# Optimization experiments

Hardware: AMD Instinct MI355X
Metric: run time of the kernel (lower is better)

The kernel has to match this reference:

```python
import jax, jax.numpy as jnp
import numpy as np

S, B = 512, 256          # seq_len, batch
A = 16                   # action_size
HID = 64                 # fc hidden_size
R = 256                  # LSTM hidden
IN = HID + A + 1         # LSTM input dim = 81


def setup_inputs() -> dict:
    key = jax.random.key(0)
    ks = jax.random.split(key, 12)
    sc = lambda fan: 1.0 / np.sqrt(fan)
    return {
        "input_tensor": jax.random.normal(ks[0], (S, B, 4, 4), jnp.float32),
        "last_action": jax.random.randint(ks[1], (S, B, 1), 0, A),
        "reward": jax.random.normal(ks[2], (S, B), jnp.float32),
        "done_flags": jax.random.bernoulli(ks[3], 0.05, (S, B)),
        "hidden_state": jax.random.normal(ks[4], (2, B, R), jnp.float32) * 0.1,
        "fc_w": jax.random.normal(ks[5], (HID, 16), jnp.float32) * sc(16),
        "fc_b": jnp.zeros((HID,), jnp.float32),
        "w_ih": jax.random.normal(ks[6], (4 * R, IN), jnp.float32) * sc(R),
        "w_hh": jax.random.normal(ks[7], (4 * R, R), jnp.float32) * sc(R),
        "b_ih": jnp.zeros((4 * R,), jnp.float32),
        "b_hh": jnp.zeros((4 * R,), jnp.float32),
        "actor_w": jax.random.normal(ks[8], (A, R), jnp.float32) * sc(R),
        "actor_b": jnp.zeros((A,), jnp.float32),
        "critic_w": jax.random.normal(ks[9], (1, R), jnp.float32) * sc(R),
        "critic_b": jnp.zeros((1,), jnp.float32),
    }


def reference(input_tensor, last_action, reward, done_flags, hidden_state,
              fc_w, fc_b, w_ih, w_hh, b_ih, b_hh,
              actor_w, actor_b, critic_w, critic_b):
    N = S * B
    # fc over flattened per-step state, then concat [fc_out, reward, one_hot(action)]
    x = input_tensor.reshape(N, 16) @ fc_w.T + fc_b                    # [N, 64]
    onehot = jax.nn.one_hot(last_action.reshape(N), A, dtype=x.dtype)  # [N, 16]
    x = jnp.concatenate([x, reward.reshape(N, 1), onehot], axis=1)     # [N, 81]
    x = x.reshape(S, B, IN)

    def step(carry, xd):
        h, c = carry                       # [B, 256] each
        xt, d = xd                          # [B, 81], [B] bool
        mask = d[:, None]
        h = jnp.where(mask, 0.0, h)         # done-flag state reset
        c = jnp.where(mask, 0.0, c)
        gates = xt @ w_ih.T + b_ih + h @ w_hh.T + b_hh   # [B, 1024]
        i, f, g, o = jnp.split(gates, 4, axis=1)          # torch LSTMCell gate order
        c = jax.nn.sigmoid(f) * c + jax.nn.sigmoid(i) * jnp.tanh(g)
        h = jax.nn.sigmoid(o) * jnp.tanh(c)
        return (h, c), h

    _, hs = jax.lax.scan(step, (hidden_state[0], hidden_state[1]), (x, done_flags))
    hs = hs.reshape(N, R)                                 # == torch.cat(lstm_outputs, 0)
    logits = hs @ actor_w.T + actor_b                     # [N, A]
    values = hs @ critic_w.T + critic_b                   # [N, 1]
    return logits.reshape(S, A, B), values.reshape(S, B)
```

## Files before the change

kernel.cpp:

```cpp
#include <hip/hip_runtime.h>
#include <hip/hip_bf16.h>

#define NS 512
#define NB 256
#define NA 16
#define NR_ 256

typedef short s16x8 __attribute__((ext_vector_type(8)));
typedef float f32x4 __attribute__((ext_vector_type(4)));

union BU { uint4 u4; unsigned short us[8]; s16x8 v; unsigned long long ull[2]; };

__device__ __forceinline__ float bf2f(unsigned short h){
  unsigned u = ((unsigned)h) << 16;
  return __builtin_bit_cast(float, u);
}
__device__ __forceinline__ unsigned short f2bf(float f){
  unsigned u = __builtin_bit_cast(unsigned, f);
  u += 0x7fffu + ((u >> 16) & 1u);
  return (unsigned short)(u >> 16);
}
__device__ __forceinline__ float fsig(float x){ return 1.f/(1.f+__expf(-x)); }
__device__ __forceinline__ float ftanh_(float x){ float e=__expf(2.f*x); return 1.f - 2.f/(e+1.f); }

__global__ void k_detect(const unsigned* __restrict__ done, unsigned* __restrict__ hdr){
  unsigned any = 0;
  for (int i = threadIdx.x; i < 32768; i += 256) any |= (done[i] > 1u) ? 1u : 0u;
  if (__ballot(any)) { if ((threadIdx.x & 63) == 0) atomicOr(hdr, 1u); }
}

__global__ void k_norm(const unsigned char* __restrict__ d8, const int* __restrict__ d32,
                       const unsigned* __restrict__ hdr, unsigned char* __restrict__ dm){
  int i = blockIdx.x*256 + threadIdx.x;
  bool u8 = (hdr[0] & 1u) != 0;
  unsigned char v;
  if (u8) v = (d8[i] != 0) ? 1 : 0; else v = (d32[i] != 0) ? 1 : 0;
  dm[i] = v;
}

__global__ void k_wbprep(const float* __restrict__ w_ih, const float* __restrict__ b_ih,
                         const float* __restrict__ b_hh, unsigned short* __restrict__ wb,
                         float* __restrict__ bsum){
  const int g = blockIdx.x*256 + threadIdx.x;
  bsum[g] = b_ih[g] + b_hh[g];
  const float* src = w_ih + (size_t)g*81;
  unsigned short* dst = wb + (size_t)g*96;
  for (int k=0;k<81;k++) dst[k]=f2bf(src[k]);
  for (int k=81;k<96;k++) dst[k]=0;
}

__global__ void k_wprep2(const float* __restrict__ w_hh, unsigned short* __restrict__ wpack){
  const int G = blockIdx.x*256 + threadIdx.x;
  const int dw  = G >> 12;
  const int rem = G & 4095;
  const int idx = rem >> 6;
  const int c   = rem & 63;
  const int lp = c >> 4, lr = c & 15;
  const int kt = idx >> 3, mt = idx & 7;
  const int grow = ((mt>>1)<<8) + (dw<<5) + ((mt&1)<<4) + lr;
  const int kcol = (kt<<5) + (lp<<3);
  const float* src = w_hh + (size_t)grow*256 + kcol;
  float4 a = *(const float4*)src;
  float4 b = *(const float4*)(src+4);
  BU u;
  u.us[0]=f2bf(a.x); u.us[1]=f2bf(a.y); u.us[2]=f2bf(a.z); u.us[3]=f2bf(a.w);
  u.us[4]=f2bf(b.x); u.us[5]=f2bf(b.y); u.us[6]=f2bf(b.z); u.us[7]=f2bf(b.w);
  *(uint4*)(wpack + (size_t)G*8) = u.u4;
}

__global__ void k_act(const float* __restrict__ input, const float* __restrict__ reward,
                      const int* __restrict__ lastact, const float* __restrict__ fc_w,
                      const float* __restrict__ fc_b, unsigned short* __restrict__ act, int n0){
  __shared__ float wf[1024];
  __shared__ float bfc[64];
  const int tid = threadIdx.x;
  for (int i=tid;i<1024;i+=256) wf[i]=fc_w[i];
  if (tid<64) bfc[tid]=fc_b[tid];
  __syncthreads();
  const int r = blockIdx.x*256 + tid;
  const int n = n0 + r;
  float in[16];
  const float4* ip = (const float4*)(input + (size_t)n*16);
  #pragma unroll
  for (int i=0;i<4;i++){ float4 v=ip[i]; in[4*i]=v.x; in[4*i+1]=v.y; in[4*i+2]=v.z; in[4*i+3]=v.w; }
  unsigned short o[96];
  const float4* wf4=(const float4*)wf;
  #pragma unroll
  for (int q=0;q<64;q++){
    float a=bfc[q];
    #pragma unroll
    for (int k4=0;k4<4;k4++){
      float4 wv=wf4[q*4+k4];
      a += in[4*k4]*wv.x + in[4*k4+1]*wv.y + in[4*k4+2]*wv.z + in[4*k4+3]*wv.w;
    }
    o[q]=f2bf(a);
  }
  o[64]=f2bf(reward[n]);
  const int la = lastact[n];
  #pragma unroll
  for (int k=0;k<16;k++) o[65+k] = (k==la) ? (unsigned short)0x3F80 : (unsigned short)0;
  #pragma unroll
  for (int k=81;k<96;k++) o[k]=0;
  uint4* dst=(uint4*)(act + (size_t)r*96);
  #pragma unroll
  for (int i=0;i<12;i++){
    BU b;
    #pragma unroll
    for (int jj=0;jj<8;jj++) b.us[jj]=o[i*8+jj];
    dst[i]=b.u4;
  }
}

__launch_bounds__(256,1) __global__ void k_gemm(
    const unsigned short* __restrict__ act, const unsigned short* __restrict__ wb,
    const float* __restrict__ bsum, unsigned short* __restrict__ xg, int mtiles){
  __shared__ __align__(16) unsigned short lA[128*104];
  __shared__ __align__(16) unsigned short lB[128*104];
  const int bm = blockIdx.x % mtiles;
  const int bn = blockIdx.x / mtiles;
  const int tid = threadIdx.x;
  {
    const int r = tid >> 1, sg = tid & 1;
    const uint4* sa = (const uint4*)(act + (size_t)(bm*128 + r)*96 + sg*48);
    const uint4* sb = (const uint4*)(wb  + (size_t)(bn*128 + r)*96 + sg*48);
    uint4* da = (uint4*)&lA[r*104 + sg*48];
    uint4* db = (uint4*)&lB[r*104 + sg*48];
    #pragma unroll
    for (int i=0;i<6;i++){ da[i]=sa[i]; db[i]=sb[i]; }
  }
  __syncthreads();
  const int wid = tid >> 6, lane = tid & 63;
  const int wm = wid >> 1, wn = wid & 1;
  const int lr = lane & 15, lp = lane >> 4;
  f32x4 acc[4][4] = {};
  #pragma unroll
  for (int kt=0;kt<3;kt++){
    s16x8 af[4], bf[4];
    #pragma unroll
    for (int mi=0;mi<4;mi++)
      af[mi] = *(const s16x8*)&lA[(wm*64 + mi*16 + lr)*104 + kt*32 + lp*8];
    #pragma unroll
    for (int ni=0;ni<4;ni++)
      bf[ni] = *(const s16x8*)&lB[(wn*64 + ni*16 + lr)*104 + kt*32 + lp*8];
    #pragma unroll
    for (int mi=0;mi<4;mi++){
      #pragma unroll
      for (int ni=0;ni<4;ni++)
        acc[mi][ni] = __builtin_amdgcn_mfma_f32_16x16x32_bf16(af[mi], bf[ni], acc[mi][ni], 0,0,0);
    }
  }
  #pragma unroll
  for (int ni=0;ni<4;ni++){
    const int col = bn*128 + wn*64 + ni*16 + lr;
    const float bias = bsum[col];
    #pragma unroll
    for (int mi=0;mi<4;mi++){
      const int row = bm*128 + wm*64 + mi*16 + lp*4;
      #pragma unroll
      for (int rr=0;rr<4;rr++)
        xg[((size_t)(row+rr)<<10) + col] = f2bf(acc[mi][ni][rr] + bias);
    }
  }
}

__launch_bounds__(512,1) __global__ void k_main(
    const float* __restrict__ hidden, const unsigned short* __restrict__ xg,
    const unsigned char* __restrict__ dm, const unsigned short* __restrict__ wpack,
    unsigned short* __restrict__ hs, float* __restrict__ cstate, int t0, int CH){
  __shared__ __align__(16) unsigned short LW[73728];
  __shared__ __align__(16) unsigned short HB[4096];
  const int tid = threadIdx.x;
  const int wg = blockIdx.x;
  const int w  = tid >> 6;
  const int lane = tid & 63;
  const int lr = lane & 15, lp = lane >> 4;
  const int bglob = (wg << 4) + lr;

  for (int it = tid; it < 9216; it += 512){
    int dw = it / 1152;
    int rem = it - dw*1152;
    *(uint4*)&LW[(size_t)dw*9216 + (size_t)rem*8] =
      *(const uint4*)(wpack + (size_t)dw*32768 + (size_t)rem*8);
  }
  s16x8 wr[46];
  #pragma unroll
  for (int f=0; f<46; ++f)
    wr[f] = *(const s16x8*)(wpack + ((size_t)(w*64 + 18 + f) << 9) + lane*8);

  {
    const int k0 = (w<<5) + (lp<<3);
    BU u;
    if (t0 == 0){
      const float* src = hidden + (size_t)bglob*256 + k0;
      float4 a = *(const float4*)src, b = *(const float4*)(src+4);
      u.us[0]=f2bf(a.x); u.us[1]=f2bf(a.y); u.us[2]=f2bf(a.z); u.us[3]=f2bf(a.w);
      u.us[4]=f2bf(b.x); u.us[5]=f2bf(b.y); u.us[6]=f2bf(b.z); u.us[7]=f2bf(b.w);
    } else {
      u.u4 = *(const uint4*)(hs + ((size_t)((CH-1)*NB + bglob) << 8) + k0);
    }
    *(uint4*)&HB[(w<<9) + ((lp<<4)+lr)*8] = u.u4;
  }
  float cst[8];
  {
    const float* csrc = (t0 == 0) ? (hidden + 65536) : cstate;
    #pragma unroll
    for (int half=0; half<2; ++half){
      float4 cv = *(const float4*)(csrc + (size_t)bglob*256 + (w<<5) + (half<<4) + (lp<<2));
      cst[half*4+0]=cv.x; cst[half*4+1]=cv.y; cst[half*4+2]=cv.z; cst[half*4+3]=cv.w;
    }
  }
  ushort4 xs[8];
  #pragma unroll
  for (int mt=0;mt<8;mt++)
    xs[mt] = *(const ushort4*)(xg + ((size_t)bglob<<10) + ((mt>>1)<<8) + (w<<5) + ((mt&1)<<4) + (lp<<2));
  bool dnc = dm[t0*NB + bglob] != 0;
  __syncthreads();

  for (int s = 0; s < CH; ++s){
    f32x4 acc[8];
    #pragma unroll
    for (int mt=0;mt<8;mt++){
      acc[mt][0]=bf2f(xs[mt].x); acc[mt][1]=bf2f(xs[mt].y);
      acc[mt][2]=bf2f(xs[mt].z); acc[mt][3]=bf2f(xs[mt].w);
    }
    const int sn = (s+1 < CH) ? (s+1) : s;
    #pragma unroll
    for (int mt=0;mt<8;mt++)
      xs[mt] = *(const ushort4*)(xg + ((size_t)(sn*NB + bglob)<<10) + ((mt>>1)<<8) + (w<<5) + ((mt&1)<<4) + (lp<<2));
    const bool dnn = dm[(t0+sn)*NB + bglob] != 0;

    #pragma unroll
    for (int kt=0;kt<8;kt++){
      BU bu; bu.u4 = *(const uint4*)&HB[(kt<<9) + lane*8];
      if (dnc) bu.u4 = make_uint4(0,0,0,0);
      #pragma unroll
      for (int mt=0;mt<8;mt++){
        const int idx = kt*8 + mt;
        s16x8 a;
        if (idx < 18) a = *(const s16x8*)&LW[w*9216 + idx*512 + lane*8];
        else          a = wr[idx-18];
        acc[mt] = __builtin_amdgcn_mfma_f32_16x16x32_bf16(a, bu.v, acc[mt], 0,0,0);
      }
    }

    unsigned short hu[8];
    #pragma unroll
    for (int half=0; half<2; ++half){
      #pragma unroll
      for (int rr=0;rr<4;rr++){
        float cp = dnc ? 0.f : cst[half*4+rr];
        float ii = fsig(acc[0+half][rr]);
        float ff = fsig(acc[2+half][rr]);
        float g2 = ftanh_(acc[4+half][rr]);
        float oo = fsig(acc[6+half][rr]);
        float cn = ff*cp + ii*g2;
        cst[half*4+rr] = cn;
        hu[half*4+rr] = f2bf(oo*ftanh_(cn));
      }
    }
    __syncthreads();
    #pragma unroll
    for (int half=0; half<2; ++half){
      unsigned long long hp = (unsigned long long)hu[half*4+0]
                            | ((unsigned long long)hu[half*4+1]<<16)
                            | ((unsigned long long)hu[half*4+2]<<32)
                            | ((unsigned long long)hu[half*4+3]<<48);
      *(unsigned long long*)&HB[(w<<9) + ((((half<<1)+(lp>>1))<<4) + lr)*8 + ((lp&1)<<2)] = hp;
      *(unsigned long long*)(hs + ((size_t)(s*NB + bglob) << 8) + (w<<5) + (half<<4) + (lp<<2)) = hp;
    }
    dnc = dnn;
    __syncthreads();
  }
  #pragma unroll
  for (int half=0; half<2; ++half)
    *(float4*)(cstate + (size_t)bglob*256 + (w<<5) + (half<<4) + (lp<<2)) =
      make_float4(cst[half*4+0], cst[half*4+1], cst[half*4+2], cst[half*4+3]);
}

__launch_bounds__(64,1) __global__ void k_proj(
    const unsigned short* __restrict__ hs, const float* __restrict__ actor_w,
    const float* __restrict__ actor_b, const float* __restrict__ critic_w,
    const float* __restrict__ critic_b, float* __restrict__ outL, float* __restrict__ outV){
  const int lane = threadIdx.x;
  const int m0 = blockIdx.x * 64;
  const int lr = lane & 15, lp = lane >> 4;
  f32x4 acc[4] = {};
  float part[4] = {0.f,0.f,0.f,0.f};
  #pragma unroll
  for (int kt=0;kt<8;kt++){
    BU bw;
    const float4* ap = (const float4*)(actor_w + (size_t)lr*256 + (kt<<5) + (lp<<3));
    float4 w0=ap[0], w1=ap[1];
    bw.us[0]=f2bf(w0.x); bw.us[1]=f2bf(w0.y); bw.us[2]=f2bf(w0.z); bw.us[3]=f2bf(w0.w);
    bw.us[4]=f2bf(w1.x); bw.us[5]=f2bf(w1.y); bw.us[6]=f2bf(w1.z); bw.us[7]=f2bf(w1.w);
    const float4* cp4 = (const float4*)(critic_w + (kt<<5) + (lp<<3));
    float4 cw0=cp4[0], cw1=cp4[1];
    #pragma unroll
    for (int mi=0;mi<4;mi++){
      BU hv; hv.u4 = *(const uint4*)(hs + ((size_t)(m0 + mi*16 + lr) << 8) + (kt<<5) + (lp<<3));
      acc[mi] = __builtin_amdgcn_mfma_f32_16x16x32_bf16(hv.v, bw.v, acc[mi], 0,0,0);
      part[mi] += bf2f(hv.us[0])*cw0.x + bf2f(hv.us[1])*cw0.y + bf2f(hv.us[2])*cw0.z + bf2f(hv.us[3])*cw0.w
                + bf2f(hv.us[4])*cw1.x + bf2f(hv.us[5])*cw1.y + bf2f(hv.us[6])*cw1.z + bf2f(hv.us[7])*cw1.w;
    }
  }
  const float ab = actor_b[lr];
  #pragma unroll
  for (int mi=0;mi<4;mi++){
    #pragma unroll
    for (int rr=0;rr<4;rr++)
      outL[(size_t)(m0 + mi*16 + lp*4 + rr)*16 + lr] = acc[mi][rr] + ab;
  }
  const float cb = critic_b[0];
  #pragma unroll
  for (int mi=0;mi<4;mi++){
    float v = part[mi];
    v += __shfl_xor(v, 16, 64);
    v += __shfl_xor(v, 32, 64);
    if (lp == 0) outV[m0 + mi*16 + lr] = v + cb;
  }
}

extern "C" void kernel_launch(void* const* d_in, const int* in_sizes, int n_in,
                              void* d_out, int out_size, void* d_ws, size_t ws_size,
                              hipStream_t stream) {
  (void)in_sizes; (void)n_in; (void)out_size;
  const float* input    = (const float*)d_in[0];
  const int*   lastact  = (const int*)d_in[1];
  const float* reward   = (const float*)d_in[2];
  const void*  done     = d_in[3];
  const float* hidden   = (const float*)d_in[4];
  const float* fc_w     = (const float*)d_in[5];
  const float* fc_b     = (const float*)d_in[6];
  const float* w_ih     = (const float*)d_in[7];
  const float* w_hh     = (const float*)d_in[8];
  const float* b_ih     = (const float*)d_in[9];
  const float* b_hh     = (const float*)d_in[10];
  const float* actor_w  = (const float*)d_in[11];
  const float* actor_b  = (const float*)d_in[12];
  const float* critic_w = (const float*)d_in[13];
  const float* critic_b = (const float*)d_in[14];
  float* outL = (float*)d_out;
  float* outV = outL + (size_t)NS*NA*NB;

  char* p = (char*)d_ws;
  unsigned*       hdr    = (unsigned*)p;
  unsigned char*  dmb    = (unsigned char*)(p + 1024);
  unsigned short* wb     = (unsigned short*)(p + 132096);
  float*          bsum   = (float*)(p + 328704);
  float*          cstate = (float*)(p + 332800);
  unsigned short* wpack  = (unsigned short*)(p + 594944);
  const size_t fixed = 1119232;
  int CH = 256;
  while (CH > 4){
    size_t need = fixed + (size_t)CH*49152 + (size_t)CH*524288 + (size_t)CH*131072;
    if (need <= ws_size) break;
    CH >>= 1;
  }
  unsigned short* act = (unsigned short*)(p + fixed);
  unsigned short* xg  = (unsigned short*)(p + fixed + (size_t)CH*49152);
  unsigned short* hs  = (unsigned short*)(p + fixed + (size_t)CH*49152 + (size_t)CH*524288);

  hipMemsetAsync(d_ws, 0, 1024, stream);
  hipLaunchKernelGGL(k_detect, dim3(1), dim3(256), 0, stream, (const unsigned*)done, hdr);
  hipLaunchKernelGGL(k_norm, dim3(512), dim3(256), 0, stream,
                     (const unsigned char*)done, (const int*)done, hdr, dmb);
  hipLaunchKernelGGL(k_wbprep, dim3(4), dim3(256), 0, stream, w_ih, b_ih, b_hh, wb, bsum);
  hipLaunchKernelGGL(k_wprep2, dim3(128), dim3(256), 0, stream, w_hh, wpack);

  const int NC = NS / CH;
  for (int c = 0; c < NC; ++c){
    const int t0 = c * CH;
    hipLaunchKernelGGL(k_act, dim3(CH), dim3(256), 0, stream,
                       input, reward, lastact, fc_w, fc_b, act, t0*NB);
    hipLaunchKernelGGL(k_gemm, dim3(CH*2*8), dim3(256), 0, stream, act, wb, bsum, xg, CH*2);
    hipLaunchKernelGGL(k_main, dim3(16), dim3(512), 0, stream,
                       hidden, xg, dmb, wpack, hs, cstate, t0, CH);
    hipLaunchKernelGGL(k_proj, dim3(CH*4), dim3(64), 0, stream,
                       hs, actor_w, actor_b, critic_w, critic_b,
                       outL + (size_t)t0*NB*NA, outV + (size_t)t0*NB);
  }
}
```

Before: 2.600 ms.

## Split LSTM gate MFMAs into two phases to cut registers and allow two blocks per CU

The recurrent gate matmul now runs in two passes of four accumulators each, for the i/g gates and then the f/o gates. The i*g product is computed between the passes, so only half the accumulators are live at once. The per-step xg prefetch into registers is dropped in favour of direct loads inside each phase, and launch bounds are raised to allow two blocks per CU. The time chunk size is also halved. The goals are lower register pressure and better occupancy or latency hiding. The cost is exposed global-load latency for xg on the serial critical path and double the HB LDS reads.

After: 3.295 ms. +26.7%, slower.

```diff
diff --git a/kernel.cpp b/kernel.cpp
--- a/kernel.cpp
+++ b/kernel.cpp
@@ -22,6 +22,10 @@
 }
 __device__ __forceinline__ float fsig(float x){ return 1.f/(1.f+__expf(-x)); }
 __device__ __forceinline__ float ftanh_(float x){ float e=__expf(2.f*x); return 1.f - 2.f/(e+1.f); }
+__device__ __forceinline__ float bfelt(ushort4 v, int i){
+  unsigned short x = (i==0)?v.x:(i==1)?v.y:(i==2)?v.z:v.w;
+  return bf2f(x);
+}
 
 __global__ void k_detect(const unsigned* __restrict__ done, unsigned* __restrict__ hdr){
   unsigned any = 0;
@@ -163,7 +167,7 @@
   }
 }
 
-__launch_bounds__(512,1) __global__ void k_main(
+__launch_bounds__(512,2) __global__ void k_main(
     const float* __restrict__ hidden, const unsigned short* __restrict__ xg,
     const unsigned char* __restrict__ dm, const unsigned short* __restrict__ wpack,
     unsigned short* __restrict__ hs, float* __restrict__ cstate, int t0, int CH){
@@ -209,51 +213,76 @@
       cst[half*4+0]=cv.x; cst[half*4+1]=cv.y; cst[half*4+2]=cv.z; cst[half*4+3]=cv.w;
     }
   }
-  ushort4 xs[8];
-  #pragma unroll
-  for (int mt=0;mt<8;mt++)
-    xs[mt] = *(const ushort4*)(xg + ((size_t)bglob<<10) + ((mt>>1)<<8) + (w<<5) + ((mt&1)<<4) + (lp<<2));
   bool dnc = dm[t0*NB + bglob] != 0;
   __syncthreads();
 
   for (int s = 0; s < CH; ++s){
-    f32x4 acc[8];
-    #pragma unroll
-    for (int mt=0;mt<8;mt++){
-      acc[mt][0]=bf2f(xs[mt].x); acc[mt][1]=bf2f(xs[mt].y);
-      acc[mt][2]=bf2f(xs[mt].z); acc[mt][3]=bf2f(xs[mt].w);
-    }
+    const unsigned short* xrow = xg + ((size_t)(s*NB + bglob) << 10) + (w<<5) + (lp<<2);
+    ushort4 xi0 = *(const ushort4*)(xrow);
+    ushort4 xi1 = *(const ushort4*)(xrow + 16);
+    ushort4 xg0 = *(const ushort4*)(xrow + 512);
+    ushort4 xg1 = *(const ushort4*)(xrow + 528);
     const int sn = (s+1 < CH) ? (s+1) : s;
-    #pragma unroll
-    for (int mt=0;mt<8;mt++)
-      xs[mt] = *(const ushort4*)(xg + ((size_t)(sn*NB + bglob)<<10) + ((mt>>1)<<8) + (w<<5) + ((mt&1)<<4) + (lp<<2));
     const bool dnn = dm[(t0+sn)*NB + bglob] != 0;
 
+    f32x4 p0={0.f,0.f,0.f,0.f}, p1=p0, p2=p0, p3=p0;
     #pragma unroll
     for (int kt=0;kt<8;kt++){
       BU bu; bu.u4 = *(const uint4*)&HB[(kt<<9) + lane*8];
       if (dnc) bu.u4 = make_uint4(0,0,0,0);
+      { const int idx = kt*8+0; s16x8 a = (idx<18)? *(const s16x8*)&LW[w*9216+idx*512+lane*8] : wr[idx-18];
+        p0 = __builtin_amdgcn_mfma_f32_16x16x32_bf16(a, bu.v, p0, 0,0,0); }
+      { const int idx = kt*8+1; s16x8 a = (idx<18)? *(const s16x8*)&LW[w*9216+idx*512+lane*8] : wr[idx-18];
+        p1 = __builtin_amdgcn_mfma_f32_16x16x32_bf16(a, bu.v, p1, 0,0,0); }
+      { const int idx = kt*8+4; s16x8 a = (idx<18)? *(const s16x8*)&LW[w*9216+idx*512+lane*8] : wr[idx-18];
+        p2 = __builtin_amdgcn_mfma_f32_16x16x32_bf16(a, bu.v, p2, 0,0,0); }
+      { const int idx = kt*8+5; s16x8 a = (idx<18)? *(const s16x8*)&LW[w*9216+idx*512+lane*8] : wr[idx-18];
+        p3 = __builtin_amdgcn_mfma_f32_16x16x32_bf16(a, bu.v, p3, 0,0,0); }
+    }
+    float u_[8];
+    #pragma unroll
+    for (int half=0; half<2; ++half){
+      f32x4 ai = half ? p1 : p0;
+      f32x4 ag_ = half ? p3 : p2;
+      ushort4 xia = half ? xi1 : xi0;
+      ushort4 xga = half ? xg1 : xg0;
       #pragma unroll
-      for (int mt=0;mt<8;mt++){
-        const int idx = kt*8 + mt;
-        s16x8 a;
-        if (idx < 18) a = *(const s16x8*)&LW[w*9216 + idx*512 + lane*8];
-        else          a = wr[idx-18];
-        acc[mt] = __builtin_amdgcn_mfma_f32_16x16x32_bf16(a, bu.v, acc[mt], 0,0,0);
-      }
+      for (int rr=0;rr<4;rr++)
+        u_[half*4+rr] = fsig(ai[rr]+bfelt(xia,rr)) * ftanh_(ag_[rr]+bfelt(xga,rr));
+    }
+
+    ushort4 xf0 = *(const ushort4*)(xrow + 256);
+    ushort4 xf1 = *(const ushort4*)(xrow + 272);
+    ushort4 xo0 = *(const ushort4*)(xrow + 768);
+    ushort4 xo1 = *(const ushort4*)(xrow + 784);
+    f32x4 q0={0.f,0.f,0.f,0.f}, q1=q0, q2=q0, q3=q0;
+    #pragma unroll
+    for (int kt=0;kt<8;kt++){
+      BU bu; bu.u4 = *(const uint4*)&HB[(kt<<9) + lane*8];
+      if (dnc) bu.u4 = make_uint4(0,0,0,0);
+      { const int idx = kt*8+2; s16x8 a = (idx<18)? *(const s16x8*)&LW[w*9216+idx*512+lane*8] : wr[idx-18];
+        q0 = __builtin_amdgcn_mfma_f32_16x16x32_bf16(a, bu.v, q0, 0,0,0); }
+      { const int idx = kt*8+3; s16x8 a = (idx<18)? *(const s16x8*)&LW[w*9216+idx*512+lane*8] : wr[idx-18];
+        q1 = __builtin_amdgcn_mfma_f32_16x16x32_bf16(a, bu.v, q1, 0,0,0); }
+      { const int idx = kt*8+6; s16x8 a = (idx<18)? *(const s16x8*)&LW[w*9216+idx*512+lane*8] : wr[idx-18];
+        q2 = __builtin_amdgcn_mfma_f32_16x16x32_bf16(a, bu.v, q2, 0,0,0); }
+      { const int idx = kt*8+7; s16x8 a = (idx<18)? *(const s16x8*)&LW[w*9216+idx*512+lane*8] : wr[idx-18];
+        q3 = __builtin_amdgcn_mfma_f32_16x16x32_bf16(a, bu.v, q3, 0,0,0); }
     }
 
     unsigned short hu[8];
     #pragma unroll
     for (int half=0; half<2; ++half){
+      f32x4 af = half ? q1 : q0;
+      f32x4 ao = half ? q3 : q2;
+      ushort4 xfa = half ? xf1 : xf0;
+      ushort4 xoa = half ? xo1 : xo0;
       #pragma unroll
       for (int rr=0;rr<4;rr++){
         float cp = dnc ? 0.f : cst[half*4+rr];
-        float ii = fsig(acc[0+half][rr]);
-        float ff = fsig(acc[2+half][rr]);
-        float g2 = ftanh_(acc[4+half][rr]);
-        float oo = fsig(acc[6+half][rr]);
-        float cn = ff*cp + ii*g2;
+        float ff = fsig(af[rr]+bfelt(xfa,rr));
+        float oo = fsig(ao[rr]+bfelt(xoa,rr));
+        float cn = ff*cp + u_[half*4+rr];
         cst[half*4+rr] = cn;
         hu[half*4+rr] = f2bf(oo*ftanh_(cn));
       }
@@ -350,7 +379,7 @@
   float*          cstate = (float*)(p + 332800);
   unsigned short* wpack  = (unsigned short*)(p + 594944);
   const size_t fixed = 1119232;
-  int CH = 256;
+  int CH = 128;
   while (CH > 4){
     size_t need = fixed + (size_t)CH*49152 + (size_t)CH*524288 + (size_t)CH*131072;
     if (need <= ws_size) break;
```

## Split LSTM step into two MFMA phases and overlap gate math with second half

Applied to the files above, without the earlier changes.

The recurrent step's MFMA work is reordered into two passes: the i/g gates first, whose activations are computed while the f/o gates' MFMAs are issued, shortening the serial critical path of each time step. The LDS weight slice shrinks to 16 k-tiles with 48 fragments held in registers, launch bounds change to allow two blocks per CU, and the x-gate loads are no longer prefetched a step ahead. The chunk size is halved. This risks register pressure or spills and exposes global-load latency for the x-gates inside each step.

Measured after the change: 3.654 ms. 40.6% more time.

```diff
diff --git a/kernel.cpp b/kernel.cpp
--- a/kernel.cpp
+++ b/kernel.cpp
@@ -163,11 +163,31 @@
   }
 }
 
-__launch_bounds__(512,1) __global__ void k_main(
+#define MFMA_ __builtin_amdgcn_mfma_f32_16x16x32_bf16
+#define LDSF(KT,MT) (*(const s16x8*)&LW2[(w<<13)+(((KT)*8+(MT))<<9)+(lane<<3)])
+#define WLOAD(KT,MT) const s16x8 wf##KT##_##MT = \
+  *(const s16x8*)(wpack + ((size_t)w<<15) + (((KT)*8+(MT))<<9) + (lane<<3));
+#define WLOADKT(KT) WLOAD(KT,0) WLOAD(KT,1) WLOAD(KT,2) WLOAD(KT,3) \
+                    WLOAD(KT,4) WLOAD(KT,5) WLOAD(KT,6) WLOAD(KT,7)
+#define QUAD(KT, B0,B1,B2,B3, A0,A1,A2,A3) { \
+  BU bu_; bu_.u4 = *(const uint4*)&HB[((KT)<<9)+(lane<<3)]; \
+  if (dnc) bu_.u4 = make_uint4(0,0,0,0); \
+  B0 = MFMA_(A0, bu_.v, B0, 0,0,0); \
+  B1 = MFMA_(A1, bu_.v, B1, 0,0,0); \
+  B2 = MFMA_(A2, bu_.v, B2, 0,0,0); \
+  B3 = MFMA_(A3, bu_.v, B3, 0,0,0); }
+#define EPI(RR, QF, QO, XF, XO, CREG, UREG, HREG) { \
+  float cp_ = dnc ? 0.f : CREG; \
+  float ff_ = fsig(QF[RR]+bf2f(XF)); \
+  float oo_ = fsig(QO[RR]+bf2f(XO)); \
+  float cn_ = ff_*cp_ + UREG; \
+  CREG = cn_; HREG = f2bf(oo_*ftanh_(cn_)); }
+
+__launch_bounds__(512,2) __global__ void k_main(
     const float* __restrict__ hidden, const unsigned short* __restrict__ xg,
     const unsigned char* __restrict__ dm, const unsigned short* __restrict__ wpack,
     unsigned short* __restrict__ hs, float* __restrict__ cstate, int t0, int CH){
-  __shared__ __align__(16) unsigned short LW[73728];
+  __shared__ __align__(16) unsigned short LW2[65536];
   __shared__ __align__(16) unsigned short HB[4096];
   const int tid = threadIdx.x;
   const int wg = blockIdx.x;
@@ -176,16 +196,11 @@
   const int lr = lane & 15, lp = lane >> 4;
   const int bglob = (wg << 4) + lr;
 
-  for (int it = tid; it < 9216; it += 512){
-    int dw = it / 1152;
-    int rem = it - dw*1152;
-    *(uint4*)&LW[(size_t)dw*9216 + (size_t)rem*8] =
-      *(const uint4*)(wpack + (size_t)dw*32768 + (size_t)rem*8);
-  }
-  s16x8 wr[46];
-  #pragma unroll
-  for (int f=0; f<46; ++f)
-    wr[f] = *(const s16x8*)(wpack + ((size_t)(w*64 + 18 + f) << 9) + lane*8);
+  for (int it = tid; it < 8192; it += 512){
+    int dw = it >> 10, rem = it & 1023;
+    *(uint4*)&LW2[(dw<<13) + rem*8] = *(const uint4*)(wpack + ((size_t)dw<<15) + rem*8);
+  }
+  WLOADKT(2) WLOADKT(3) WLOADKT(4) WLOADKT(5) WLOADKT(6) WLOADKT(7)
 
   {
     const int k0 = (w<<5) + (lp<<3);
@@ -200,81 +215,82 @@
     }
     *(uint4*)&HB[(w<<9) + ((lp<<4)+lr)*8] = u.u4;
   }
-  float cst[8];
+  float c0,c1,c2,c3,c4,c5,c6,c7;
   {
     const float* csrc = (t0 == 0) ? (hidden + 65536) : cstate;
-    #pragma unroll
-    for (int half=0; half<2; ++half){
-      float4 cv = *(const float4*)(csrc + (size_t)bglob*256 + (w<<5) + (half<<4) + (lp<<2));
-      cst[half*4+0]=cv.x; cst[half*4+1]=cv.y; cst[half*4+2]=cv.z; cst[half*4+3]=cv.w;
-    }
-  }
-  ushort4 xs[8];
-  #pragma unroll
-  for (int mt=0;mt<8;mt++)
-    xs[mt] = *(const ushort4*)(xg + ((size_t)bglob<<10) + ((mt>>1)<<8) + (w<<5) + ((mt&1)<<4) + (lp<<2));
-  bool dnc = dm[t0*NB + bglob] != 0;
+    float4 cv0 = *(const float4*)(csrc + (size_t)bglob*256 + (w<<5) + (lp<<2));
+    float4 cv1 = *(const float4*)(csrc + (size_t)bglob*256 + (w<<5) + 16 + (lp<<2));
+    c0=cv0.x; c1=cv0.y; c2=cv0.z; c3=cv0.w;
+    c4=cv1.x; c5=cv1.y; c6=cv1.z; c7=cv1.w;
+  }
   __syncthreads();
 
   for (int s = 0; s < CH; ++s){
-    f32x4 acc[8];
-    #pragma unroll
-    for (int mt=0;mt<8;mt++){
-      acc[mt][0]=bf2f(xs[mt].x); acc[mt][1]=bf2f(xs[mt].y);
-      acc[mt][2]=bf2f(xs[mt].z); acc[mt][3]=bf2f(xs[mt].w);
-    }
-    const int sn = (s+1 < CH) ? (s+1) : s;
-    #pragma unroll
-    for (int mt=0;mt<8;mt++)
-      xs[mt] = *(const ushort4*)(xg + ((size_t)(sn*NB + bglob)<<10) + ((mt>>1)<<8) + (w<<5) + ((mt&1)<<4) + (lp<<2));
-    const bool dnn = dm[(t0+sn)*NB + bglob] != 0;
-
-    #pragma unroll
-    for (int kt=0;kt<8;kt++){
-      BU bu; bu.u4 = *(const uint4*)&HB[(kt<<9) + lane*8];
-      if (dnc) bu.u4 = make_uint4(0,0,0,0);
-      #pragma unroll
-      for (int mt=0;mt<8;mt++){
-        const int idx = kt*8 + mt;
-        s16x8 a;
-        if (idx < 18) a = *(const s16x8*)&LW[w*9216 + idx*512 + lane*8];
-        else          a = wr[idx-18];
-        acc[mt] = __builtin_amdgcn_mfma_f32_16x16x32_bf16(a, bu.v, acc[mt], 0,0,0);
-      }
-    }
-
-    unsigned short hu[8];
-    #pragma unroll
-    for (int half=0; half<2; ++half){
-      #pragma unroll
-      for (int rr=0;rr<4;rr++){
-        float cp = dnc ? 0.f : cst[half*4+rr];
-        float ii = fsig(acc[0+half][rr]);
-        float ff = fsig(acc[2+half][rr]);
-        float g2 = ftanh_(acc[4+half][rr]);
-        float oo = fsig(acc[6+half][rr]);
-        float cn = ff*cp + ii*g2;
-        cst[half*4+rr] = cn;
-        hu[half*4+rr] = f2bf(oo*ftanh_(cn));
-      }
-    }
+    const bool dnc = dm[(t0+s)*NB + bglob] != 0;
+    const unsigned short* xrow = xg + ((size_t)(s*NB + bglob) << 10) + (w<<5) + (lp<<2);
+    ushort4 xi0 = *(const ushort4*)(xrow);
+    ushort4 xi1 = *(const ushort4*)(xrow + 16);
+    ushort4 xG0 = *(const ushort4*)(xrow + 512);
+    ushort4 xG1 = *(const ushort4*)(xrow + 528);
+
+    f32x4 p0={0.f,0.f,0.f,0.f}, p1=p0, p2=p0, p3=p0;
+    QUAD(0, p0,p1,p2,p3, LDSF(0,0), LDSF(0,1), LDSF(0,4), LDSF(0,5))
+    QUAD(1, p0,p1,p2,p3, LDSF(1,0), LDSF(1,1), LDSF(1,4), LDSF(1,5))
+    QUAD(2, p0,p1,p2,p3, wf2_0, wf2_1, wf2_4, wf2_5)
+    QUAD(3, p0,p1,p2,p3, wf3_0, wf3_1, wf3_4, wf3_5)
+    QUAD(4, p0,p1,p2,p3, wf4_0, wf4_1, wf4_4, wf4_5)
+    QUAD(5, p0,p1,p2,p3, wf5_0, wf5_1, wf5_4, wf5_5)
+    QUAD(6, p0,p1,p2,p3, wf6_0, wf6_1, wf6_4, wf6_5)
+    QUAD(7, p0,p1,p2,p3, wf7_0, wf7_1, wf7_4, wf7_5)
+
+    float u0 = fsig(p0[0]+bf2f(xi0.x)) * ftanh_(p2[0]+bf2f(xG0.x));
+    float u1 = fsig(p0[1]+bf2f(xi0.y)) * ftanh_(p2[1]+bf2f(xG0.y));
+    float u2 = fsig(p0[2]+bf2f(xi0.z)) * ftanh_(p2[2]+bf2f(xG0.z));
+    float u3 = fsig(p0[3]+bf2f(xi0.w)) * ftanh_(p2[3]+bf2f(xG0.w));
+    float u4 = fsig(p1[0]+bf2f(xi1.x)) * ftanh_(p3[0]+bf2f(xG1.x));
+    float u5 = fsig(p1[1]+bf2f(xi1.y)) * ftanh_(p3[1]+bf2f(xG1.y));
+    float u6 = fsig(p1[2]+bf2f(xi1.z)) * ftanh_(p3[2]+bf2f(xG1.z));
+    float u7 = fsig(p1[3]+bf2f(xi1.w)) * ftanh_(p3[3]+bf2f(xG1.w));
+
+    ushort4 xf0 = *(const ushort4*)(xrow + 256);
+    ushort4 xf1 = *(const ushort4*)(xrow + 272);
+    ushort4 xo0 = *(const ushort4*)(xrow + 768);
+    ushort4 xo1 = *(const ushort4*)(xrow + 784);
+    f32x4 q0={0.f,0.f,0.f,0.f}, q1=q0, q2=q0, q3=q0;
+    QUAD(0, q0,q1,q2,q3, LDSF(0,2), LDSF(0,3), LDSF(0,6), LDSF(0,7))
+    QUAD(1, q0,q1,q2,q3, LDSF(1,2), LDSF(1,3), LDSF(1,6), LDSF(1,7))
+    QUAD(2, q0,q1,q2,q3, wf2_2, wf2_3, wf2_6, wf2_7)
+    QUAD(3, q0,q1,q2,q3, wf3_2, wf3_3, wf3_6, wf3_7)
+    QUAD(4, q0,q1,q2,q3, wf4_2, wf4_3, wf4_6, wf4_7)
+    QUAD(5, q0,q1,q2,q3, wf5_2, wf5_3, wf5_6, wf5_7)
+    QUAD(6, q0,q1,q2,q3, wf6_2, wf6_3, wf6_6, wf6_7)
+    QUAD(7, q0,q1,q2,q3, wf7_2, wf7_3, wf7_6, wf7_7)
+
+    unsigned short h0,h1,h2,h3,h4,h5,h6,h7;
+    EPI(0, q0,q2, xf0.x, xo0.x, c0, u0, h0)
+    EPI(1, q0,q2, xf0.y, xo0.y, c1, u1, h1)
+    EPI(2, q0,q2, xf0.z, xo0.z, c2, u2, h2)
+    EPI(3, q0,q2, xf0.w, xo0.w, c3, u3, h3)
+    EPI(0, q1,q3, xf1.x, xo1.x, c4, u4, h4)
+    EPI(1, q1,q3, xf1.y, xo1.y, c5, u5, h5)
+    EPI(2, q1,q3, xf1.z, xo1.z, c6, u6, h6)
+    EPI(3, q1,q3, xf1.w, xo1.w, c7, u7, h7)
+
     __syncthreads();
-    #pragma unroll
-    for (int half=0; half<2; ++half){
-      unsigned long long hp = (unsigned long long)hu[half*4+0]
-                            | ((unsigned long long)hu[half*4+1]<<16)
-                            | ((unsigned long long)hu[half*4+2]<<32)
-                            | ((unsigned long long)hu[half*4+3]<<48);
-      *(unsigned long long*)&HB[(w<<9) + ((((half<<1)+(lp>>1))<<4) + lr)*8 + ((lp&1)<<2)] = hp;
-      *(unsigned long long*)(hs + ((size_t)(s*NB + bglob) << 8) + (w<<5) + (half<<4) + (lp<<2)) = hp;
-    }
-    dnc = dnn;
+    unsigned long long hpA = (unsigned long long)h0 | ((unsigned long long)h1<<16)
+                           | ((unsigned long long)h2<<32) | ((unsigned long long)h3<<48);
+    unsigned long long hpB = (unsigned long long)h4 | ((unsigned long long)h5<<16)
+                           | ((unsigned long long)h6<<32) | ((unsigned long long)h7<<48);
+    *(unsigned long long*)&HB[(w<<9) + (((lp>>1)<<4) + lr)*8 + ((lp&1)<<2)] = hpA;
+    *(unsigned long long*)&HB[(w<<9) + (((2+(lp>>1))<<4) + lr)*8 + ((lp&1)<<2)] = hpB;
+    unsigned long long* hdst =
+      (unsigned long long*)(hs + ((size_t)(s*NB + bglob) << 8) + (w<<5) + (lp<<2));
+    hdst[0] = hpA;
+    hdst[4] = hpB;
     __syncthreads();
   }
-  #pragma unroll
-  for (int half=0; half<2; ++half)
-    *(float4*)(cstate + (size_t)bglob*256 + (w<<5) + (half<<4) + (lp<<2)) =
-      make_float4(cst[half*4+0], cst[half*4+1], cst[half*4+2], cst[half*4+3]);
+  *(float4*)(cstate + (size_t)bglob*256 + (w<<5) + (lp<<2)) = make_float4(c0,c1,c2,c3);
+  *(float4*)(cstate + (size_t)bglob*256 + (w<<5) + 16 + (lp<<2)) = make_float4(c4,c5,c6,c7);
 }
 
 __launch_bounds__(64,1) __global__ void k_proj(
@@ -350,7 +366,7 @@
   float*          cstate = (float*)(p + 332800);
   unsigned short* wpack  = (unsigned short*)(p + 594944);
   const size_t fixed = 1119232;
-  int CH = 256;
+  int CH = 128;
   while (CH > 4){
     size_t need = fixed + (size_t)CH*49152 + (size_t)CH*524288 + (size_t)CH*131072;
     if (need <= ws_size) break;
```
